# Kernel optimization log

Hardware: AMD Instinct MI355X
Metric: run time of the kernel (lower is better)

The kernel has to match this reference:

```python
import jax, jax.numpy as jnp
from jax import lax
import numpy as np

EPS = 1e-5


def _fps(xyz, S):
    B, N, _ = xyz.shape

    def step(carry, _):
        dist, far = carry  # [B,N], [B]
        c = xyz[jnp.arange(B), far]               # [B,3]
        d = jnp.sum((xyz - c[:, None, :]) ** 2, -1)  # [B,N]
        dist = jnp.minimum(dist, d)
        nxt = jnp.argmax(dist, -1).astype(jnp.int32)
        return (dist, nxt), far

    init = (jnp.full((B, N), 1e10, xyz.dtype), jnp.zeros((B,), jnp.int32))
    _, idxs = lax.scan(step, init, None, length=S)
    return jnp.transpose(idxs)  # [B,S]


def _gather(pts, idx):
    # pts: [B,N,C], idx: [B,...] -> [B,...,C]
    return jax.vmap(lambda p, i: p[i])(pts, idx)


def _conv(x, W, b):
    # 1x1 Conv1d: x [M,Cin,L], W [Cout,Cin], b [Cout]
    return jnp.einsum('mcl,oc->mol', x, W) + b[None, :, None]


def _bn(x, g, b):
    # BatchNorm1d (training-mode batch stats, biased variance)
    mu = jnp.mean(x, (0, 2), keepdims=True)
    v = jnp.var(x, (0, 2), keepdims=True)
    return g[None, :, None] * (x - mu) / jnp.sqrt(v + EPS) + b[None, :, None]


def _forward(xyz, feature, affine_alpha, affine_beta, w_tr, b_tr, g_tr, be_tr,
             w1, b1, g1, be1, w2, b2, groups, k):
    xyz = jnp.transpose(xyz, (0, 2, 1))        # [B,N,3]
    feature = jnp.transpose(feature, (0, 2, 1))  # [B,N,D]
    B, N, _ = xyz.shape
    S = groups
    xyz_ng = lax.stop_gradient(xyz)  # cluster() runs under torch.no_grad
    fps_idx = _fps(xyz_ng, S)                        # [B,S]
    new_xyz = _gather(xyz_ng, fps_idx)               # [B,S,3] (detached)
    # squared-distance kNN: [B,S,N]
    sqr = (jnp.sum(new_xyz ** 2, -1)[:, :, None]
           + jnp.sum(xyz_ng ** 2, -1)[:, None, :]
           - 2.0 * jnp.einsum('bsc,bnc->bsn', new_xyz, xyz_ng))
    _, idx = lax.top_k(-sqr, k)                      # [B,S,k] smallest distances
    new_feature = _gather(feature, fps_idx)          # [B,S,D]
    grouped_xyz = _gather(xyz, idx)                  # [B,S,k,3]
    grouped_feature = _gather(feature, idx)          # [B,S,k,D]
    grouped_feature = jnp.concatenate([grouped_feature, grouped_xyz], -1)  # [B,S,k,D+3]
    # anchor normalization
    mean = jnp.concatenate([new_feature, new_xyz], -1)[:, :, None, :]  # [B,S,1,D+3]
    diff = grouped_feature - mean
    std = jnp.std(diff.reshape(B, -1), axis=-1, ddof=1)[:, None, None, None]
    gf = affine_alpha * (diff / (std + EPS)) + affine_beta
    # concat anchor feature -> [B,S,k,2D+3]
    D = new_feature.shape[-1]
    x = jnp.concatenate([gf, jnp.broadcast_to(new_feature[:, :, None, :], (B, S, k, D))], -1)
    d = x.shape[-1]
    # PreExtraction: [B,S,k,d] -> [B*S,d,k]
    x = jnp.transpose(x, (0, 1, 3, 2)).reshape(B * S, d, k)
    x = jax.nn.relu(_bn(_conv(x, w_tr, b_tr), g_tr, be_tr))
    y = jax.nn.relu(_bn(_conv(x, w1, b1), g1, be1))
    y = _conv(y, w2, b2)
    x = jax.nn.relu(y + x)
    x = jnp.max(x, -1).reshape(B, S, -1)             # adaptive_max_pool1d(1)
    return (jnp.transpose(new_xyz, (0, 2, 1)), jnp.transpose(x, (0, 2, 1)))


def setup_inputs() -> dict:
    key = jax.random.key(0)
    k0, k1, k2, k3, k4 = jax.random.split(key, 5)
    B, N, D = 8, 4096, 64
    return {
        'xyz': jax.random.normal(k0, (B, 3, N), jnp.float32),
        'feature': jax.random.normal(k1, (B, D, N), jnp.float32),
        'affine_alpha': jnp.ones((1, 1, 1, D + 3), jnp.float32),
        'affine_beta': jnp.zeros((1, 1, 1, D + 3), jnp.float32),
        'w_tr': 0.05 * jax.random.normal(k2, (D, 3 + 2 * D), jnp.float32),
        'b_tr': jnp.zeros((D,), jnp.float32),
        'g_tr': jnp.ones((D,), jnp.float32),
        'be_tr': jnp.zeros((D,), jnp.float32),
        'w1': 0.05 * jax.random.normal(k3, (D, D), jnp.float32),
        'b1': jnp.zeros((D,), jnp.float32),
        'g1': jnp.ones((D,), jnp.float32),
        'be1': jnp.zeros((D,), jnp.float32),
        'w2': 0.05 * jax.random.normal(k4, (D, D), jnp.float32),
        'b2': jnp.zeros((D,), jnp.float32),
        'groups': 1024,
        'k': 32,
    }


def reference(xyz, feature, affine_alpha, affine_beta, w_tr, b_tr, g_tr, be_tr,
              w1, b1, g1, be1, w2, b2, groups, k):
    return _forward(xyz, feature, affine_alpha, affine_beta, w_tr, b_tr, g_tr, be_tr,
                    w1, b1, g1, be1, w2, b2, groups, k)
```

## Files before the change

### kernel.cpp

```cpp
#include <hip/hip_runtime.h>
#include <cfloat>
#include <math.h>

#define B_ 8
#define N_ 4096
#define D_ 64
#define S_ 1024
#define K_ 32
#define CIN_ 131

template <int CTRL>
__device__ __forceinline__ unsigned long long dpp_u64(unsigned long long k) {
  int lo = (int)(unsigned int)k, hi = (int)(unsigned int)(k >> 32);
  lo = __builtin_amdgcn_update_dpp(lo, lo, CTRL, 0xf, 0xf, false);
  hi = __builtin_amdgcn_update_dpp(hi, hi, CTRL, 0xf, 0xf, false);
  return ((unsigned long long)(unsigned int)hi << 32) | (unsigned int)lo;
}

__device__ __forceinline__ float wave_max_f32_dpp(float v) {
  int x = __float_as_int(v);
#define STEP(ctrl)                                                        \
  {                                                                       \
    int t = __builtin_amdgcn_update_dpp(x, x, ctrl, 0xf, 0xf, false);     \
    v = fmaxf(v, __int_as_float(t));                                      \
    x = __float_as_int(v);                                                \
  }
  STEP(0x111)
  STEP(0x112)
  STEP(0x114)
  STEP(0x118)
  STEP(0x142)
  STEP(0x143)
#undef STEP
  return __int_as_float(__builtin_amdgcn_readlane(x, 63));
}

__device__ __forceinline__ void wait_count(const unsigned int* p, unsigned int val) {
  while (__hip_atomic_load(p, __ATOMIC_ACQUIRE, __HIP_MEMORY_SCOPE_AGENT) < val)
    __builtin_amdgcn_s_sleep(8);
}
__device__ __forceinline__ void rel_add(unsigned int* p) {
  __hip_atomic_fetch_add(p, 1u, __ATOMIC_RELEASE, __HIP_MEMORY_SCOPE_AGENT);
}

__global__ __launch_bounds__(256) void stage1_kernel(
    const float* __restrict__ xyz, const float* __restrict__ feature,
    int* __restrict__ fps_idx, float* __restrict__ nxyz, float* __restrict__ out0,
    float* __restrict__ featT, int* __restrict__ knn, float* __restrict__ nfeat,
    float* __restrict__ dcache, float* __restrict__ outp,
    unsigned int* __restrict__ flags, unsigned int* __restrict__ kcount,
    unsigned int* __restrict__ gcount, unsigned int* __restrict__ tcount) {
  const int bid = blockIdx.x, tid = threadIdx.x;
  __shared__ __align__(16) float4 sp[N_];
  __shared__ int si64[64];
  __shared__ unsigned long long kbuf[2][4];

  if (bid < 8) {
    const int b = bid;
    const float* xb = xyz + (size_t)b * 3 * N_;
    const float4* xv = (const float4*)xb;
    float px[16], py[16], pz[16], dist[16];
#pragma unroll
    for (int q = 0; q < 4; q++) {
      float4 X = xv[4 * tid + q];
      float4 Y = xv[1024 + 4 * tid + q];
      float4 Z = xv[2048 + 4 * tid + q];
      px[4 * q + 0] = X.x; px[4 * q + 1] = X.y; px[4 * q + 2] = X.z; px[4 * q + 3] = X.w;
      py[4 * q + 0] = Y.x; py[4 * q + 1] = Y.y; py[4 * q + 2] = Y.z; py[4 * q + 3] = Y.w;
      pz[4 * q + 0] = Z.x; pz[4 * q + 1] = Z.y; pz[4 * q + 2] = Z.z; pz[4 * q + 3] = Z.w;
    }
#pragma unroll
    for (int i = 0; i < 16; i++) {
      dist[i] = 1e10f;
      sp[16 * tid + i] = make_float4(px[i], py[i], pz[i], 0.f);
    }
    if (tid == 0) si64[0] = 0;
    __syncthreads();
    float cx = sp[0].x, cy = sp[0].y, cz = sp[0].z;
    const int wav = tid >> 6, lane = tid & 63;
    for (int s = 1; s < S_; s++) {
      float best = -1.0f;
      int bi = 16 * tid;
#pragma unroll
      for (int i = 0; i < 16; i++) {
        float dx = __fsub_rn(px[i], cx);
        float dy = __fsub_rn(py[i], cy);
        float dz = __fsub_rn(pz[i], cz);
        float d = __fadd_rn(__fadd_rn(__fmul_rn(dx, dx), __fmul_rn(dy, dy)), __fmul_rn(dz, dz));
        dist[i] = fminf(dist[i], d);
        if (dist[i] > best) { best = dist[i]; bi = 16 * tid + i; }
      }
      float wmax = wave_max_f32_dpp(best);
      unsigned long long m = __ballot(best == wmax);
      int l = __ffsll(m) - 1;
      int widx = __builtin_amdgcn_readlane(bi, l);
      if (lane == 0)
        kbuf[s & 1][wav] =
            ((unsigned long long)(unsigned int)__float_as_int(wmax) << 32) |
            (unsigned int)(4095 - widx);
      __syncthreads();
      unsigned long long k = kbuf[s & 1][lane & 3];
      unsigned long long t;
      t = dpp_u64<0xB1>(k); if (t > k) k = t;
      t = dpp_u64<0x4E>(k); if (t > k) k = t;
      int bix = 4095 - (int)(k & 0xfffull);
      if (tid == 0) si64[s & 63] = bix;
      float4 c = sp[bix];
      cx = c.x; cy = c.y; cz = c.z;
      if ((s & 63) == 63) {
        __syncthreads();
        if (tid < 64) {
          int ss = (s - 63) + tid;
          int gs = b * S_ + ss;
          int n = si64[tid];
          float4 cc = sp[n];
          fps_idx[gs] = n;
          nxyz[(size_t)gs * 3 + 0] = cc.x;
          nxyz[(size_t)gs * 3 + 1] = cc.y;
          nxyz[(size_t)gs * 3 + 2] = cc.z;
          out0[(size_t)b * 3 * S_ + ss] = cc.x;
          out0[(size_t)b * 3 * S_ + S_ + ss] = cc.y;
          out0[(size_t)b * 3 * S_ + 2 * S_ + ss] = cc.z;
        }
        __syncthreads();
        if (tid == 0) {
          __threadfence();
          __hip_atomic_store(&flags[b * 16 + (s >> 6)], 1u, __ATOMIC_RELEASE,
                             __HIP_MEMORY_SCOPE_AGENT);
        }
      }
    }
    return;
  }
  if (bid < 520) {
    const int blk = bid - 8;
    const int b = blk >> 6, n0 = (blk & 63) * 64;
    float* tile = (float*)sp;
#pragma unroll
    for (int i = 0; i < 16; i++) {
      int c = i * 4 + (tid >> 6), nl = tid & 63;
      tile[c * 65 + nl] = feature[((size_t)b * 64 + c) * N_ + n0 + nl];
    }
    __syncthreads();
#pragma unroll
    for (int i = 0; i < 16; i++) {
      int nl = i * 4 + (tid >> 6), c = tid & 63;
      featT[((size_t)b * N_ + n0 + nl) * 64 + c] = tile[c * 65 + nl];
    }
    __syncthreads();
    if (tid == 0) rel_add(tcount);
    return;
  }
  if (bid < 8712) {
    const int bs = bid - 520;
    if (tid == 0) wait_count(&flags[bs >> 6], 1);
    __syncthreads();
    const int b = bs >> 10;
    const float* xb = xyz + (size_t)b * 3 * N_;
    const float cx = nxyz[(size_t)bs * 3], cy = nxyz[(size_t)bs * 3 + 1],
                cz = nxyz[(size_t)bs * 3 + 2];
    const float cn = __fadd_rn(__fadd_rn(__fmul_rn(cx, cx), __fmul_rn(cy, cy)), __fmul_rn(cz, cz));
    float d[16];
#pragma unroll
    for (int i = 0; i < 16; i++) {
      int n = i * 256 + tid;
      float px = xb[n], py = xb[N_ + n], pz = xb[2 * N_ + n];
      float pn = __fadd_rn(__fadd_rn(__fmul_rn(px, px), __fmul_rn(py, py)), __fmul_rn(pz, pz));
      float dot = __fadd_rn(__fadd_rn(__fmul_rn(cx, px), __fmul_rn(cy, py)), __fmul_rn(cz, pz));
      d[i] = __fsub_rn(__fadd_rn(cn, pn), __fmul_rn(2.0f, dot));
    }
    float mv = FLT_MAX;
    int mi = tid;
#pragma unroll
    for (int i = 0; i < 16; i++)
      if (d[i] < mv) { mv = d[i]; mi = i * 256 + tid; }
    int* skk = si64;
    const int wav = tid >> 6, lane = tid & 63;
    for (int j = 0; j < K_; j++) {
      unsigned int u = __float_as_uint(mv);
      u ^= ((unsigned int)((int)u >> 31) | 0x80000000u);
      unsigned long long key = ((unsigned long long)u << 32) | (unsigned int)mi;
#pragma unroll
      for (int off = 32; off >= 1; off >>= 1) {
        unsigned long long ok = __shfl_xor(key, off);
        if (ok < key) key = ok;
      }
      if (lane == 0) kbuf[j & 1][wav] = key;
      __syncthreads();
      unsigned long long kmin = kbuf[j & 1][0];
#pragma unroll
      for (int w = 1; w < 4; w++) {
        unsigned long long k2 = kbuf[j & 1][w];
        if (k2 < kmin) kmin = k2;
      }
      int g = (int)(kmin & 0xffffffffull);
      if (tid == 0) skk[j] = g;
      if ((g & 255) == tid) {
        int sl = g >> 8;
#pragma unroll
        for (int i = 0; i < 16; i++)
          if (i == sl) d[i] = FLT_MAX;
        mv = FLT_MAX; mi = tid;
#pragma unroll
        for (int i = 0; i < 16; i++)
          if (d[i] < mv) { mv = d[i]; mi = i * 256 + tid; }
      }
    }
    __syncthreads();
    if (tid < K_) knn[(size_t)bs * K_ + tid] = skk[tid];
    __syncthreads();
    if (tid == 0) rel_add(&kcount[bs >> 6]);
    return;
  }
  if (bid < 10760) {
    const int j = bid - 8712;
    if (tid == 0) {
      wait_count(tcount, 512);
      wait_count(&flags[j >> 4], 1);
    }
    __syncthreads();
    int e = j * 256 + tid;
    int bsx = e >> 6, c = e & 63;
    int bq = bsx >> 10;
    int n = fps_idx[bsx];
    nfeat[e] = featT[((size_t)bq * N_ + n) * 64 + c];
    __syncthreads();
    if (tid == 0) rel_add(&gcount[j >> 4]);
    return;
  }
  {
    const int blk = bid - 10760;
    if (tid == 0) {
      wait_count(tcount, 512);
      wait_count(&kcount[blk >> 3], 64);
      wait_count(&gcount[blk >> 3], 16);
    }
    __syncthreads();
    int* sk = si64;
    float s = 0.f, q = 0.f;
    const int c = tid & 63, qd = tid >> 6;
    for (int g = 0; g < 8; g++) {
      const int bs = blk * 8 + g, b = bs >> 10;
      if (tid < 32) sk[tid] = knn[(size_t)bs * K_ + tid];
      __syncthreads();
      float anc = nfeat[(size_t)bs * 64 + c];
#pragma unroll
      for (int it = 0; it < 8; it++) {
        int kk = it * 4 + qd;
        int n = sk[kk];
        float dd = featT[((size_t)b * N_ + n) * 64 + c] - anc;
        s += dd; q += dd * dd;
        dcache[((size_t)bs * 32 + kk) * 68 + c] = dd;
      }
      if (tid < 96) {
        int c3 = tid >> 5, kk = tid & 31;
        int n = sk[kk];
        float dd = xyz[((size_t)b * 3 + c3) * N_ + n] - nxyz[(size_t)bs * 3 + c3];
        s += dd; q += dd * dd;
        dcache[((size_t)bs * 32 + kk) * 68 + 64 + c3] = dd;
      }
      __syncthreads();
    }
#pragma unroll
    for (int off = 32; off >= 1; off >>= 1) { s += __shfl_xor(s, off); q += __shfl_xor(q, off); }
    float* rs = (float*)kbuf;
    float* rq = rs + 4;
    if ((tid & 63) == 0) { rs[tid >> 6] = s; rq[tid >> 6] = q; }
    __syncthreads();
    if (tid == 0) {
      outp[blk * 2] = rs[0] + rs[1] + rs[2] + rs[3];
      outp[blk * 2 + 1] = rq[0] + rq[1] + rq[2] + rq[3];
    }
  }
}

__global__ __launch_bounds__(256) void fps_kernel(const float* __restrict__ xyz,
                                                  int* __restrict__ fps_idx,
                                                  float* __restrict__ nxyz,
                                                  float* __restrict__ out0) {
  const int tid = threadIdx.x;
  __shared__ __align__(16) float4 sp[N_];
  __shared__ int si[S_];
  __shared__ unsigned long long keyp[2][4];
  const int b = blockIdx.x;
  const float* xb = xyz + (size_t)b * 3 * N_;
  const float4* xv = (const float4*)xb;
  float px[16], py[16], pz[16], dist[16];
#pragma unroll
  for (int q = 0; q < 4; q++) {
    float4 X = xv[4 * tid + q];
    float4 Y = xv[1024 + 4 * tid + q];
    float4 Z = xv[2048 + 4 * tid + q];
    px[4 * q + 0] = X.x; px[4 * q + 1] = X.y; px[4 * q + 2] = X.z; px[4 * q + 3] = X.w;
    py[4 * q + 0] = Y.x; py[4 * q + 1] = Y.y; py[4 * q + 2] = Y.z; py[4 * q + 3] = Y.w;
    pz[4 * q + 0] = Z.x; pz[4 * q + 1] = Z.y; pz[4 * q + 2] = Z.z; pz[4 * q + 3] = Z.w;
  }
#pragma unroll
  for (int i = 0; i < 16; i++) {
    dist[i] = 1e10f;
    sp[16 * tid + i] = make_float4(px[i], py[i], pz[i], 0.f);
  }
  if (tid == 0) si[0] = 0;
  __syncthreads();
  float cx = sp[0].x, cy = sp[0].y, cz = sp[0].z;
  const int wav = tid >> 6, lane = tid & 63;
  for (int s = 1; s < S_; s++) {
    float best = -1.0f;
    int bi = 16 * tid;
#pragma unroll
    for (int i = 0; i < 16; i++) {
      float dx = __fsub_rn(px[i], cx);
      float dy = __fsub_rn(py[i], cy);
      float dz = __fsub_rn(pz[i], cz);
      float d = __fadd_rn(__fadd_rn(__fmul_rn(dx, dx), __fmul_rn(dy, dy)), __fmul_rn(dz, dz));
      dist[i] = fminf(dist[i], d);
      if (dist[i] > best) { best = dist[i]; bi = 16 * tid + i; }
    }
    float wmax = wave_max_f32_dpp(best);
    unsigned long long m = __ballot(best == wmax);
    int l = __ffsll(m) - 1;
    int widx = __builtin_amdgcn_readlane(bi, l);
    if (lane == 0)
      keyp[s & 1][wav] =
          ((unsigned long long)(unsigned int)__float_as_int(wmax) << 32) |
          (unsigned int)(4095 - widx);
    __syncthreads();
    unsigned long long k = keyp[s & 1][lane & 3];
    unsigned long long t;
    t = dpp_u64<0xB1>(k); if (t > k) k = t;
    t = dpp_u64<0x4E>(k); if (t > k) k = t;
    int bix = 4095 - (int)(k & 0xfffull);
    if (tid == 0) si[s] = bix;
    float4 c = sp[bix];
    cx = c.x; cy = c.y; cz = c.z;
  }
  __syncthreads();
  for (int e = tid; e < S_; e += 256) {
    int n = si[e];
    fps_idx[b * S_ + e] = n;
    float4 c = sp[n];
    nxyz[(size_t)(b * S_ + e) * 3 + 0] = c.x;
    nxyz[(size_t)(b * S_ + e) * 3 + 1] = c.y;
    nxyz[(size_t)(b * S_ + e) * 3 + 2] = c.z;
    out0[(size_t)b * 3 * S_ + e] = c.x;
    out0[(size_t)b * 3 * S_ + S_ + e] = c.y;
    out0[(size_t)b * 3 * S_ + 2 * S_ + e] = c.z;
  }
}

__global__ __launch_bounds__(256) void knn_kernel(const float* __restrict__ xyz,
                                                  const float* __restrict__ nxyz,
                                                  int* __restrict__ knn) {
  const int bs = blockIdx.x, tid = threadIdx.x;
  const int b = bs >> 10;
  const float* xb = xyz + (size_t)b * 3 * N_;
  const float cx = nxyz[(size_t)bs * 3], cy = nxyz[(size_t)bs * 3 + 1], cz = nxyz[(size_t)bs * 3 + 2];
  const float cn = __fadd_rn(__fadd_rn(__fmul_rn(cx, cx), __fmul_rn(cy, cy)), __fmul_rn(cz, cz));
  float d[16];
#pragma unroll
  for (int i = 0; i < 16; i++) {
    int n = i * 256 + tid;
    float px = xb[n], py = xb[N_ + n], pz = xb[2 * N_ + n];
    float pn = __fadd_rn(__fadd_rn(__fmul_rn(px, px), __fmul_rn(py, py)), __fmul_rn(pz, pz));
    float dot = __fadd_rn(__fadd_rn(__fmul_rn(cx, px), __fmul_rn(cy, py)), __fmul_rn(cz, pz));
    d[i] = __fsub_rn(__fadd_rn(cn, pn), __fmul_rn(2.0f, dot));
  }
  float mv = FLT_MAX;
  int mi = tid;
#pragma unroll
  for (int i = 0; i < 16; i++)
    if (d[i] < mv) { mv = d[i]; mi = i * 256 + tid; }
  __shared__ unsigned long long keyp[2][4];
  __shared__ int skk[K_];
  const int wav = tid >> 6, lane = tid & 63;
  for (int j = 0; j < K_; j++) {
    unsigned int u = __float_as_uint(mv);
    u ^= ((unsigned int)((int)u >> 31) | 0x80000000u);
    unsigned long long key = ((unsigned long long)u << 32) | (unsigned int)mi;
#pragma unroll
    for (int off = 32; off >= 1; off >>= 1) {
      unsigned long long ok = __shfl_xor(key, off);
      if (ok < key) key = ok;
    }
    if (lane == 0) keyp[j & 1][wav] = key;
    __syncthreads();
    unsigned long long kmin = keyp[j & 1][0];
#pragma unroll
    for (int w = 1; w < 4; w++) {
      unsigned long long k2 = keyp[j & 1][w];
      if (k2 < kmin) kmin = k2;
    }
    int g = (int)(kmin & 0xffffffffull);
    if (tid == 0) skk[j] = g;
    if ((g & 255) == tid) {
      int sl = g >> 8;
#pragma unroll
      for (int i = 0; i < 16; i++)
        if (i == sl) d[i] = FLT_MAX;
      mv = FLT_MAX; mi = tid;
#pragma unroll
      for (int i = 0; i < 16; i++)
        if (d[i] < mv) { mv = d[i]; mi = i * 256 + tid; }
    }
  }
  __syncthreads();
  if (tid < K_) knn[(size_t)bs * K_ + tid] = skk[tid];
}

__global__ __launch_bounds__(256) void gather_nf(const float* __restrict__ feature,
                                                 const int* __restrict__ fps_i,
                                                 float* __restrict__ nfeat) {
  int e = blockIdx.x * 256 + threadIdx.x;
  int b = e >> 16, rem = e & 65535;
  int s = rem >> 6, c = rem & 63;
  int n = fps_i[b * S_ + s];
  nfeat[e] = feature[((size_t)b * 64 + c) * N_ + n];
}

__global__ __launch_bounds__(256) void std_partial(const float* __restrict__ feature,
                                                   const float* __restrict__ xyz,
                                                   const float* __restrict__ nxyz,
                                                   const float* __restrict__ nfeat,
                                                   const int* __restrict__ knn,
                                                   float* __restrict__ outp) {
  const int blk = blockIdx.x, tid = threadIdx.x;
  const int b = blk >> 6, chunk = blk & 63;
  float s = 0.f, q = 0.f;
  for (int e = tid; e < 16 * K_ * 67; e += 256) {
    int so = e / (K_ * 67);
    int rem = e - so * (K_ * 67);
    int kk = rem / 67;
    int c = rem - kk * 67;
    int bs = b * S_ + chunk * 16 + so;
    int n = knn[(size_t)bs * K_ + kk];
    float raw = (c < 64) ? feature[((size_t)b * 64 + c) * N_ + n]
                         : xyz[((size_t)b * 3 + (c - 64)) * N_ + n];
    float anc = (c < 64) ? nfeat[(size_t)bs * 64 + c]
                         : nxyz[(size_t)bs * 3 + (c - 64)];
    float dd = raw - anc;
    s += dd; q += dd * dd;
  }
#pragma unroll
  for (int off = 32; off >= 1; off >>= 1) { s += __shfl_xor(s, off); q += __shfl_xor(q, off); }
  __shared__ float rs[4], rq[4];
  if ((tid & 63) == 0) { rs[tid >> 6] = s; rq[tid >> 6] = q; }
  __syncthreads();
  if (tid == 0) {
    outp[blk * 2] = rs[0] + rs[1] + rs[2] + rs[3];
    outp[blk * 2 + 1] = rq[0] + rq[1] + rq[2] + rq[3];
  }
}

__global__ void std_final(const float* __restrict__ part, float* __restrict__ invstd) {
  int b = threadIdx.x;
  if (b < B_) {
    double s = 0.0, q = 0.0;
    for (int i = 0; i < 64; i++) {
      s += (double)part[(b * 64 + i) * 2];
      q += (double)part[(b * 64 + i) * 2 + 1];
    }
    const double n = (double)(S_ * K_ * 67);
    double var = (q - s * s / n) / (n - 1.0);
    invstd[b] = (float)(1.0 / (sqrt(var) + 1e-5));
  }
}

template <int MODE>
__global__ __launch_bounds__(256, 2) void mlp_kernel(
    const float* __restrict__ feature, const float* __restrict__ xyz,
    const float* __restrict__ nxyz, const float* __restrict__ nfeat,
    const int* __restrict__ knn, const float* __restrict__ invstd,
    const float* __restrict__ alpha, const float* __restrict__ beta,
    const float* __restrict__ w_tr, const float* __restrict__ b_tr,
    const float* __restrict__ w1, const float* __restrict__ b1,
    const float* __restrict__ w2, const float* __restrict__ b2,
    const float* __restrict__ bn_tr, const float* __restrict__ bn_1,
    float* __restrict__ bnpart, float* __restrict__ out1) {
  __shared__ __align__(16) float pool[15556];
  float* Wt = pool;
  float* xin = pool + 8516;
  float* ub = xin;
  float* tb = pool + 8516 + 4192;
  float* part = pool + 8516 + 4192 + 2304;
  int* sknn = (int*)(part + 512);
  const int bs = blockIdx.x, tid = threadIdx.x;
  const int b = bs >> 10, s = bs & 1023;
  if (tid < K_) sknn[tid] = knn[(size_t)bs * K_ + tid];
  for (int e = tid; e < 64 * 131; e += 256) {
    int o = e / 131, c = e - o * 131;
    Wt[c * 65 + o] = w_tr[e];
  }
  __syncthreads();
  const float inv = invstd[b];
  for (int e = tid; e < CIN_ * K_; e += 256) {
    int c = e >> 5, kk = e & 31;
    float v;
    if (c < 67) {
      int n = sknn[kk];
      float raw = (c < 64) ? feature[((size_t)b * 64 + c) * N_ + n]
                           : xyz[((size_t)b * 3 + (c - 64)) * N_ + n];
      float anc = (c < 64) ? nfeat[(size_t)bs * 64 + c]
                           : nxyz[(size_t)bs * 3 + (c - 64)];
      v = alpha[c] * ((raw - anc) * inv) + beta[c];
    } else {
      v = nfeat[(size_t)bs * 64 + (c - 67)];
    }
    xin[e] = v;
  }
  __syncthreads();
  const int o = tid & 63, kkb = (tid >> 6) * 8;
  float acc[8];
  {
    float bv = b_tr[o];
#pragma unroll
    for (int j = 0; j < 8; j++) acc[j] = bv;
  }
  for (int c = 0; c < CIN_; c++) {
    float w = Wt[c * 65 + o];
    const float4 xa = *(const float4*)(xin + c * 32 + kkb);
    const float4 xb4 = *(const float4*)(xin + c * 32 + kkb + 4);
    acc[0] += w * xa.x; acc[1] += w * xa.y; acc[2] += w * xa.z; acc[3] += w * xa.w;
    acc[4] += w * xb4.x; acc[5] += w * xb4.y; acc[6] += w * xb4.z; acc[7] += w * xb4.w;
  }
  if (MODE == 0) {
    float s8 = 0.f, q8 = 0.f;
#pragma unroll
    for (int j = 0; j < 8; j++) { s8 += acc[j]; q8 += acc[j] * acc[j]; }
    part[(tid >> 6) * 64 + o] = s8;
    part[256 + (tid >> 6) * 64 + o] = q8;
    __syncthreads();
    if (tid < 64) {
      float ss = 0.f, qq = 0.f;
      for (int g = 0; g < 4; g++) { ss += part[g * 64 + tid]; qq += part[256 + g * 64 + tid]; }
      bnpart[(size_t)bs * 128 + tid] = ss;
      bnpart[(size_t)bs * 128 + 64 + tid] = qq;
    }
    return;
  }
  float tv[8];
  {
    float sc = bn_tr[o], sh = bn_tr[64 + o];
#pragma unroll
    for (int j = 0; j < 8; j++) {
      tv[j] = fmaxf(fmaf(sc, acc[j], sh), 0.f);
      tb[o * 36 + kkb + j] = tv[j];
    }
  }
  __syncthreads();
  for (int e = tid; e < 64 * 64; e += 256) {
    int oo = e >> 6, c = e & 63;
    Wt[c * 65 + oo] = w1[e];
  }
  __syncthreads();
  float acc2[8];
  {
    float bv = b1[o];
#pragma unroll
    for (int j = 0; j < 8; j++) acc2[j] = bv;
  }
  for (int c = 0; c < 64; c++) {
    float w = Wt[c * 65 + o];
    const float4 ta = *(const float4*)(tb + c * 36 + kkb);
    const float4 ta2 = *(const float4*)(tb + c * 36 + kkb + 4);
    acc2[0] += w * ta.x; acc2[1] += w * ta.y; acc2[2] += w * ta.z; acc2[3] += w * ta.w;
    acc2[4] += w * ta2.x; acc2[5] += w * ta2.y; acc2[6] += w * ta2.z; acc2[7] += w * ta2.w;
  }
  if (MODE == 1) {
    float s8 = 0.f, q8 = 0.f;
#pragma unroll
    for (int j = 0; j < 8; j++) { s8 += acc2[j]; q8 += acc2[j] * acc2[j]; }
    part[(tid >> 6) * 64 + o] = s8;
    part[256 + (tid >> 6) * 64 + o] = q8;
    __syncthreads();
    if (tid < 64) {
      float ss = 0.f, qq = 0.f;
      for (int g = 0; g < 4; g++) { ss += part[g * 64 + tid]; qq += part[256 + g * 64 + tid]; }
      bnpart[(size_t)bs * 128 + tid] = ss;
      bnpart[(size_t)bs * 128 + 64 + tid] = qq;
    }
    return;
  }
  {
    float sc = bn_1[o], sh = bn_1[64 + o];
#pragma unroll
    for (int j = 0; j < 8; j++) ub[o * 36 + kkb + j] = fmaxf(fmaf(sc, acc2[j], sh), 0.f);
  }
  __syncthreads();
  for (int e = tid; e < 64 * 64; e += 256) {
    int oo = e >> 6, c = e & 63;
    Wt[c * 65 + oo] = w2[e];
  }
  __syncthreads();
  float acc3[8];
  {
    float bv = b2[o];
#pragma unroll
    for (int j = 0; j < 8; j++) acc3[j] = bv;
  }
  for (int c = 0; c < 64; c++) {
    float w = Wt[c * 65 + o];
    const float4 ua = *(const float4*)(ub + c * 36 + kkb);
    const float4 ua2 = *(const float4*)(ub + c * 36 + kkb + 4);
    acc3[0] += w * ua.x; acc3[1] += w * ua.y; acc3[2] += w * ua.z; acc3[3] += w * ua.w;
    acc3[4] += w * ua2.x; acc3[5] += w * ua2.y; acc3[6] += w * ua2.z; acc3[7] += w * ua2.w;
  }
  float m = 0.f;
#pragma unroll
  for (int j = 0; j < 8; j++) m = fmaxf(m, fmaxf(acc3[j] + tv[j], 0.f));
  part[(tid >> 6) * 64 + o] = m;
  __syncthreads();
  if (tid < 64) {
    float mm = part[tid];
    for (int g = 1; g < 4; g++) mm = fmaxf(mm, part[g * 64 + tid]);
    out1[((size_t)b * 64 + tid) * S_ + s] = mm;
  }
}

__global__ __launch_bounds__(256) void bn_finalize(const float* __restrict__ part,
                                                   const float* __restrict__ g,
                                                   const float* __restrict__ be,
                                                   float* __restrict__ bnout) {
  const int ch = blockIdx.x, tid = threadIdx.x;
  double s = 0.0, q = 0.0;
  for (int i = tid; i < B_ * S_; i += 256) {
    s += (double)part[(size_t)i * 128 + ch];
    q += (double)part[(size_t)i * 128 + 64 + ch];
  }
#pragma unroll
  for (int off = 32; off >= 1; off >>= 1) { s += __shfl_xor(s, off); q += __shfl_xor(q, off); }
  __shared__ double ls[4], lq[4];
  if ((tid & 63) == 0) { ls[tid >> 6] = s; lq[tid >> 6] = q; }
  __syncthreads();
  if (tid == 0) {
    double Ssum = ls[0] + ls[1] + ls[2] + ls[3];
    double Qsum = lq[0] + lq[1] + lq[2] + lq[3];
    const double n = (double)(B_ * S_ * K_);
    double mu = Ssum / n;
    double var = Qsum / n - mu * mu;
    double sc = (double)g[ch] / sqrt(var + 1e-5);
    bnout[ch] = (float)sc;
    bnout[64 + ch] = (float)((double)be[ch] - mu * sc);
  }
}

__global__ void std_final_c(const float* __restrict__ part, float* __restrict__ invstd) {
  int b = threadIdx.x;
  if (b < B_) {
    double s = 0.0, q = 0.0;
    for (int i = 0; i < 128; i++) {
      s += (double)part[(b * 128 + i) * 2];
      q += (double)part[(b * 128 + i) * 2 + 1];
    }
    const double n = (double)(S_ * K_ * 67);
    double var = (q - s * s / n) / (n - 1.0);
    invstd[b] = (float)(1.0 / (sqrt(var) + 1e-5));
  }
}

__global__ __launch_bounds__(256, 2) void mlp0c(
    const float* __restrict__ dcache, const float* __restrict__ nfeat,
    const float* __restrict__ invstd,
    const float* __restrict__ alpha, const float* __restrict__ beta,
    const float* __restrict__ w_tr, const float* __restrict__ b_tr,
    float* __restrict__ bnpart, float* __restrict__ tcache) {
  __shared__ __align__(16) float pool[13220];
  float* Wt = pool;
  float* xin = pool + 8516;
  float* part = pool + 8516 + 4192;
  const int bs = blockIdx.x, tid = threadIdx.x;
  const int b = bs >> 10;
  for (int e = tid; e < 64 * 131; e += 256) {
    int o = e / 131, c = e - o * 131;
    Wt[c * 65 + o] = w_tr[e];
  }
  const float inv = invstd[b];
  {
    const int c = tid & 63, qd = tid >> 6;
    float al = alpha[c], bev = beta[c];
#pragma unroll
    for (int it = 0; it < 8; it++) {
      int kk = it * 4 + qd;
      xin[c * 32 + kk] = al * (dcache[((size_t)bs * 32 + kk) * 68 + c] * inv) + bev;
    }
    if (tid < 96) {
      int c3 = 64 + (tid >> 5), kk = tid & 31;
      xin[c3 * 32 + kk] =
          alpha[c3] * (dcache[((size_t)bs * 32 + kk) * 68 + c3] * inv) + beta[c3];
    }
    for (int e = tid; e < 2048; e += 256) {
      int cc = 67 + (e >> 5), kk = e & 31;
      xin[cc * 32 + kk] = nfeat[(size_t)bs * 64 + (e >> 5)];
    }
  }
  __syncthreads();
  const int o = tid & 63, kkb = (tid >> 6) * 8;
  float acc[8];
  {
    float bv = b_tr[o];
#pragma unroll
    for (int j = 0; j < 8; j++) acc[j] = bv;
  }
  for (int c = 0; c < CIN_; c++) {
    float w = Wt[c * 65 + o];
    const float4 xa = *(const float4*)(xin + c * 32 + kkb);
    const float4 xb4 = *(const float4*)(xin + c * 32 + kkb + 4);
    acc[0] += w * xa.x; acc[1] += w * xa.y; acc[2] += w * xa.z; acc[3] += w * xa.w;
    acc[4] += w * xb4.x; acc[5] += w * xb4.y; acc[6] += w * xb4.z; acc[7] += w * xb4.w;
  }
  {
    float4* tp = (float4*)(tcache + ((size_t)bs * 64 + o) * 32 + kkb);
    tp[0] = make_float4(acc[0], acc[1], acc[2], acc[3]);
    tp[1] = make_float4(acc[4], acc[5], acc[6], acc[7]);
  }
  float s8 = 0.f, q8 = 0.f;
#pragma unroll
  for (int j = 0; j < 8; j++) { s8 += acc[j]; q8 += acc[j] * acc[j]; }
  part[(tid >> 6) * 64 + o] = s8;
  part[256 + (tid >> 6) * 64 + o] = q8;
  __syncthreads();
  if (tid < 64) {
    float ss = 0.f, qq = 0.f;
    for (int g = 0; g < 4; g++) { ss += part[g * 64 + tid]; qq += part[256 + g * 64 + tid]; }
    bnpart[(size_t)bs * 128 + tid] = ss;
    bnpart[(size_t)bs * 128 + 64 + tid] = qq;
  }
}

__global__ __launch_bounds__(256, 3) void mlp1c(
    const float* __restrict__ tcache, const float* __restrict__ bn_tr,
    const float* __restrict__ w1, const float* __restrict__ b1,
    float* __restrict__ bnpart, float* __restrict__ ucache) {
  __shared__ __align__(16) float pool[6976];
  float* Wt = pool;
  float* tb = pool + 4160;
  float* part = pool + 4160 + 2304;
  const int bs = blockIdx.x, tid = threadIdx.x;
  const int o = tid & 63, kkb = (tid >> 6) * 8;
  for (int e = tid; e < 64 * 64; e += 256) {
    int oo = e >> 6, c = e & 63;
    Wt[c * 65 + oo] = w1[e];
  }
  float t[8];
  {
    const float4* tp = (const float4*)(tcache + ((size_t)bs * 64 + o) * 32 + kkb);
    float4 a = tp[0], b4 = tp[1];
    t[0] = a.x; t[1] = a.y; t[2] = a.z; t[3] = a.w;
    t[4] = b4.x; t[5] = b4.y; t[6] = b4.z; t[7] = b4.w;
  }
  {
    float sc = bn_tr[o], sh = bn_tr[64 + o];
#pragma unroll
    for (int j = 0; j < 8; j++) tb[o * 36 + kkb + j] = fmaxf(fmaf(sc, t[j], sh), 0.f);
  }
  __syncthreads();
  float acc2[8];
  {
    float bv = b1[o];
#pragma unroll
    for (int j = 0; j < 8; j++) acc2[j] = bv;
  }
  for (int c = 0; c < 64; c++) {
    float w = Wt[c * 65 + o];
    const float4 ta = *(const float4*)(tb + c * 36 + kkb);
    const float4 ta2 = *(const float4*)(tb + c * 36 + kkb + 4);
    acc2[0] += w * ta.x; acc2[1] += w * ta.y; acc2[2] += w * ta.z; acc2[3] += w * ta.w;
    acc2[4] += w * ta2.x; acc2[5] += w * ta2.y; acc2[6] += w * ta2.z; acc2[7] += w * ta2.w;
  }
  {
    float4* up = (float4*)(ucache + ((size_t)bs * 64 + o) * 32 + kkb);
    up[0] = make_float4(acc2[0], acc2[1], acc2[2], acc2[3]);
    up[1] = make_float4(acc2[4], acc2[5], acc2[6], acc2[7]);
  }
  float s8 = 0.f, q8 = 0.f;
#pragma unroll
  for (int j = 0; j < 8; j++) { s8 += acc2[j]; q8 += acc2[j] * acc2[j]; }
  part[(tid >> 6) * 64 + o] = s8;
  part[256 + (tid >> 6) * 64 + o] = q8;
  __syncthreads();
  if (tid < 64) {
    float ss = 0.f, qq = 0.f;
    for (int g = 0; g < 4; g++) { ss += part[g * 64 + tid]; qq += part[256 + g * 64 + tid]; }
    bnpart[(size_t)bs * 128 + tid] = ss;
    bnpart[(size_t)bs * 128 + 64 + tid] = qq;
  }
}

__global__ __launch_bounds__(256, 3) void mlp2c(
    const float* __restrict__ tcache, const float* __restrict__ ucache,
    const float* __restrict__ bn_tr, const float* __restrict__ bn_1,
    const float* __restrict__ w2, const float* __restrict__ b2,
    float* __restrict__ out1) {
  __shared__ __align__(16) float pool[6976];
  float* Wt = pool;
  float* ub = pool + 4160;
  float* part = pool + 4160 + 2304;
  const int bs = blockIdx.x, tid = threadIdx.x;
  const int b = bs >> 10, s = bs & 1023;
  const int o = tid & 63, kkb = (tid >> 6) * 8;
  for (int e = tid; e < 64 * 64; e += 256) {
    int oo = e >> 6, c = e & 63;
    Wt[c * 65 + oo] = w2[e];
  }
  {
    const float4* up = (const float4*)(ucache + ((size_t)bs * 64 + o) * 32 + kkb);
    float4 a = up[0], b4 = up[1];
    float u[8] = {a.x, a.y, a.z, a.w, b4.x, b4.y, b4.z, b4.w};
    float sc = bn_1[o], sh = bn_1[64 + o];
#pragma unroll
    for (int j = 0; j < 8; j++) ub[o * 36 + kkb + j] = fmaxf(fmaf(sc, u[j], sh), 0.f);
  }
  __syncthreads();
  float acc3[8];
  {
    float bv = b2[o];
#pragma unroll
    for (int j = 0; j < 8; j++) acc3[j] = bv;
  }
  for (int c = 0; c < 64; c++) {
    float w = Wt[c * 65 + o];
    const float4 ua = *(const float4*)(ub + c * 36 + kkb);
    const float4 ua2 = *(const float4*)(ub + c * 36 + kkb + 4);
    acc3[0] += w * ua.x; acc3[1] += w * ua.y; acc3[2] += w * ua.z; acc3[3] += w * ua.w;
    acc3[4] += w * ua2.x; acc3[5] += w * ua2.y; acc3[6] += w * ua2.z; acc3[7] += w * ua2.w;
  }
  float tv[8];
  {
    const float4* tp = (const float4*)(tcache + ((size_t)bs * 64 + o) * 32 + kkb);
    float4 a = tp[0], b4 = tp[1];
    float t[8] = {a.x, a.y, a.z, a.w, b4.x, b4.y, b4.z, b4.w};
    float sc = bn_tr[o], sh = bn_tr[64 + o];
#pragma unroll
    for (int j = 0; j < 8; j++) tv[j] = fmaxf(fmaf(sc, t[j], sh), 0.f);
  }
  float m = 0.f;
#pragma unroll
  for (int j = 0; j < 8; j++) m = fmaxf(m, fmaxf(acc3[j] + tv[j], 0.f));
  part[(tid >> 6) * 64 + o] = m;
  __syncthreads();
  if (tid < 64) {
    float mm = part[tid];
    for (int g = 1; g < 4; g++) mm = fmaxf(mm, part[g * 64 + tid]);
    out1[((size_t)b * 64 + tid) * S_ + s] = mm;
  }
}

extern "C" void kernel_launch(void* const* d_in, const int* in_sizes, int n_in,
                              void* d_out, int out_size, void* d_ws, size_t ws_size,
                              hipStream_t stream) {
  const float* xyz = (const float*)d_in[0];
  const float* feature = (const float*)d_in[1];
  const float* alpha = (const float*)d_in[2];
  const float* beta = (const float*)d_in[3];
  const float* w_tr = (const float*)d_in[4];
  const float* b_tr = (const float*)d_in[5];
  const float* g_tr = (const float*)d_in[6];
  const float* be_tr = (const float*)d_in[7];
  const float* w1 = (const float*)d_in[8];
  const float* b1 = (const float*)d_in[9];
  const float* g1 = (const float*)d_in[10];
  const float* be1 = (const float*)d_in[11];
  const float* w2 = (const float*)d_in[12];
  const float* b2 = (const float*)d_in[13];

  char* ws = (char*)d_ws;
  int* fps_i = (int*)(ws);
  float* nxyz = (float*)(ws + 32768);
  float* nfeat = (float*)(ws + 131072);
  int* knn = (int*)(ws + 2228224);
  float* stdpart = (float*)(ws + 3276800);
  float* invstd = (float*)(ws + 3280896);
  float* bn_tr = (float*)(ws + 3280960);
  float* bn_1 = (float*)(ws + 3281472);
  float* bnpart = (float*)(ws + 3281984);
  float* featT = (float*)(ws + 7476288);
  float* dcache = (float*)(ws + 15864896);
  float* tcache = (float*)(ws + 87168064);
  float* ucache = (float*)(ws + 154276928);
  float* stdpart_c = (float*)(ws + 221385792);
  unsigned int* flags = (unsigned int*)(ws + 221393984);
  unsigned int* kcount = (unsigned int*)(ws + 221394496);
  unsigned int* gcount = (unsigned int*)(ws + 221395008);
  unsigned int* tcount = (unsigned int*)(ws + 221395520);

  float* out0 = (float*)d_out;
  float* out1 = out0 + B_ * 3 * S_;

  const bool big = (ws_size >= 221395584ull);

  if (big) {
    hipMemsetAsync(ws + 221393984, 0, 1600, stream);
    stage1_kernel<<<8 + 512 + 8192 + 2048 + 1024, 256, 0, stream>>>(
        xyz, feature, fps_i, nxyz, out0, featT, knn, nfeat, dcache, stdpart_c,
        flags, kcount, gcount, tcount);
    std_final_c<<<1, 64, 0, stream>>>(stdpart_c, invstd);
    mlp0c<<<B_ * S_, 256, 0, stream>>>(dcache, nfeat, invstd, alpha, beta, w_tr, b_tr,
                                       bnpart, tcache);
    bn_finalize<<<64, 256, 0, stream>>>(bnpart, g_tr, be_tr, bn_tr);
    mlp1c<<<B_ * S_, 256, 0, stream>>>(tcache, bn_tr, w1, b1, bnpart, ucache);
    bn_finalize<<<64, 256, 0, stream>>>(bnpart, g1, be1, bn_1);
    mlp2c<<<B_ * S_, 256, 0, stream>>>(tcache, ucache, bn_tr, bn_1, w2, b2, out1);
  } else {
    fps_kernel<<<8, 256, 0, stream>>>(xyz, fps_i, nxyz, out0);
    gather_nf<<<(B_ * S_ * D_) / 256, 256, 0, stream>>>(feature, fps_i, nfeat);
    knn_kernel<<<8192, 256, 0, stream>>>(xyz, nxyz, knn);
    std_partial<<<B_ * 64, 256, 0, stream>>>(feature, xyz, nxyz, nfeat, knn, stdpart);
    std_final<<<1, 64, 0, stream>>>(stdpart, invstd);
    mlp_kernel<0><<<B_ * S_, 256, 0, stream>>>(feature, xyz, nxyz, nfeat, knn, invstd,
                                               alpha, beta, w_tr, b_tr, w1, b1, w2, b2,
                                               bn_tr, bn_1, bnpart, out1);
    bn_finalize<<<64, 256, 0, stream>>>(bnpart, g_tr, be_tr, bn_tr);
    mlp_kernel<1><<<B_ * S_, 256, 0, stream>>>(feature, xyz, nxyz, nfeat, knn, invstd,
                                               alpha, beta, w_tr, b_tr, w1, b1, w2, b2,
                                               bn_tr, bn_1, bnpart, out1);
    bn_finalize<<<64, 256, 0, stream>>>(bnpart, g1, be1, bn_1);
    mlp_kernel<2><<<B_ * S_, 256, 0, stream>>>(feature, xyz, nxyz, nfeat, knn, invstd,
                                               alpha, beta, w_tr, b_tr, w1, b1, w2, b2,
                                               bn_tr, bn_1, bnpart, out1);
  }
}
```

Baseline: 1.402 ms.

## Carry FPS winner coordinates through reductions and shrink shared memory footprint

The FPS loop now tracks the coordinates of each thread's farthest point and forwards them through the wave and cross-wave reductions via LDS and DPP. This removes the per-iteration dependent LDS lookup of the chosen point, so the 64KB per-point LDS array can be dropped. Shared memory shrinks to a roughly 16KB pool, which should let more blocks of the other stages share a CU. The spin-wait also polls with relaxed loads and issues a single acquire after it exits. The trade-off is extra DPP moves and LDS stores on every FPS iteration.

```diff
diff --git a/kernel.cpp b/kernel.cpp
--- a/kernel.cpp
+++ b/kernel.cpp
@@ -15,6 +15,12 @@
   lo = __builtin_amdgcn_update_dpp(lo, lo, CTRL, 0xf, 0xf, false);
   hi = __builtin_amdgcn_update_dpp(hi, hi, CTRL, 0xf, 0xf, false);
   return ((unsigned long long)(unsigned int)hi << 32) | (unsigned int)lo;
+}
+
+template <int CTRL>
+__device__ __forceinline__ float dpp_f32(float v) {
+  int t = __builtin_amdgcn_update_dpp(__float_as_int(v), __float_as_int(v), CTRL, 0xf, 0xf, false);
+  return __int_as_float(t);
 }
 
 __device__ __forceinline__ float wave_max_f32_dpp(float v) {
@@ -36,8 +42,9 @@
 }
 
 __device__ __forceinline__ void wait_count(const unsigned int* p, unsigned int val) {
-  while (__hip_atomic_load(p, __ATOMIC_ACQUIRE, __HIP_MEMORY_SCOPE_AGENT) < val)
+  while (__hip_atomic_load(p, __ATOMIC_RELAXED, __HIP_MEMORY_SCOPE_AGENT) < val)
     __builtin_amdgcn_s_sleep(8);
+  (void)__hip_atomic_load(p, __ATOMIC_ACQUIRE, __HIP_MEMORY_SCOPE_AGENT);
 }
 __device__ __forceinline__ void rel_add(unsigned int* p) {
   __hip_atomic_fetch_add(p, 1u, __ATOMIC_RELEASE, __HIP_MEMORY_SCOPE_AGENT);
@@ -51,9 +58,11 @@
     unsigned int* __restrict__ flags, unsigned int* __restrict__ kcount,
     unsigned int* __restrict__ gcount, unsigned int* __restrict__ tcount) {
   const int bid = blockIdx.x, tid = threadIdx.x;
-  __shared__ __align__(16) float4 sp[N_];
-  __shared__ int si64[64];
-  __shared__ unsigned long long kbuf[2][4];
+  __shared__ __align__(16) float pool[4160];
+  float4* scoord64 = (float4*)pool;
+  int* si64 = (int*)(pool + 256);
+  unsigned long long* kbuf = (unsigned long long*)(pool + 320);
+  float4* cbuf = (float4*)(pool + 336);
 
   if (bid < 8) {
     const int b = bid;
@@ -70,17 +79,19 @@
       pz[4 * q + 0] = Z.x; pz[4 * q + 1] = Z.y; pz[4 * q + 2] = Z.z; pz[4 * q + 3] = Z.w;
     }
 #pragma unroll
-    for (int i = 0; i < 16; i++) {
-      dist[i] = 1e10f;
-      sp[16 * tid + i] = make_float4(px[i], py[i], pz[i], 0.f);
-    }
-    if (tid == 0) si64[0] = 0;
-    __syncthreads();
-    float cx = sp[0].x, cy = sp[0].y, cz = sp[0].z;
+    for (int i = 0; i < 16; i++) dist[i] = 1e10f;
+    if (tid == 0) {
+      si64[0] = 0;
+      scoord64[0] = make_float4(px[0], py[0], pz[0], 0.f);
+    }
+    __syncthreads();
+    float4 c0 = scoord64[0];
+    float cx = c0.x, cy = c0.y, cz = c0.z;
     const int wav = tid >> 6, lane = tid & 63;
     for (int s = 1; s < S_; s++) {
       float best = -1.0f;
       int bi = 16 * tid;
+      float bx = px[0], by = py[0], bz = pz[0];
 #pragma unroll
       for (int i = 0; i < 16; i++) {
         float dx = __fsub_rn(px[i], cx);
@@ -88,39 +99,51 @@
         float dz = __fsub_rn(pz[i], cz);
         float d = __fadd_rn(__fadd_rn(__fmul_rn(dx, dx), __fmul_rn(dy, dy)), __fmul_rn(dz, dz));
         dist[i] = fminf(dist[i], d);
-        if (dist[i] > best) { best = dist[i]; bi = 16 * tid + i; }
+        if (dist[i] > best) {
+          best = dist[i]; bi = 16 * tid + i;
+          bx = px[i]; by = py[i]; bz = pz[i];
+        }
       }
       float wmax = wave_max_f32_dpp(best);
       unsigned long long m = __ballot(best == wmax);
       int l = __ffsll(m) - 1;
-      int widx = __builtin_amdgcn_readlane(bi, l);
-      if (lane == 0)
-        kbuf[s & 1][wav] =
-            ((unsigned long long)(unsigned int)__float_as_int(wmax) << 32) |
-            (unsigned int)(4095 - widx);
+      if (lane == l) {
+        kbuf[(s & 1) * 4 + wav] =
+            ((unsigned long long)(unsigned int)__float_as_int(best) << 32) |
+            (unsigned int)(4095 - bi);
+        cbuf[(s & 1) * 4 + wav] = make_float4(bx, by, bz, 0.f);
+      }
       __syncthreads();
-      unsigned long long k = kbuf[s & 1][lane & 3];
-      unsigned long long t;
-      t = dpp_u64<0xB1>(k); if (t > k) k = t;
-      t = dpp_u64<0x4E>(k); if (t > k) k = t;
+      unsigned long long k = kbuf[(s & 1) * 4 + (lane & 3)];
+      float4 cc = cbuf[(s & 1) * 4 + (lane & 3)];
+      {
+        unsigned long long t = dpp_u64<0xB1>(k);
+        float tx = dpp_f32<0xB1>(cc.x), ty = dpp_f32<0xB1>(cc.y), tz = dpp_f32<0xB1>(cc.z);
+        if (t > k) { k = t; cc.x = tx; cc.y = ty; cc.z = tz; }
+        t = dpp_u64<0x4E>(k);
+        tx = dpp_f32<0x4E>(cc.x); ty = dpp_f32<0x4E>(cc.y); tz = dpp_f32<0x4E>(cc.z);
+        if (t > k) { k = t; cc.x = tx; cc.y = ty; cc.z = tz; }
+      }
       int bix = 4095 - (int)(k & 0xfffull);
-      if (tid == 0) si64[s & 63] = bix;
-      float4 c = sp[bix];
-      cx = c.x; cy = c.y; cz = c.z;
+      cx = cc.x; cy = cc.y; cz = cc.z;
+      if (tid == 0) {
+        si64[s & 63] = bix;
+        scoord64[s & 63] = make_float4(cx, cy, cz, 0.f);
+      }
       if ((s & 63) == 63) {
         __syncthreads();
         if (tid < 64) {
           int ss = (s - 63) + tid;
           int gs = b * S_ + ss;
           int n = si64[tid];
-          float4 cc = sp[n];
+          float4 cc2 = scoord64[tid];
           fps_idx[gs] = n;
-          nxyz[(size_t)gs * 3 + 0] = cc.x;
-          nxyz[(size_t)gs * 3 + 1] = cc.y;
-          nxyz[(size_t)gs * 3 + 2] = cc.z;
-          out0[(size_t)b * 3 * S_ + ss] = cc.x;
-          out0[(size_t)b * 3 * S_ + S_ + ss] = cc.y;
-          out0[(size_t)b * 3 * S_ + 2 * S_ + ss] = cc.z;
+          nxyz[(size_t)gs * 3 + 0] = cc2.x;
+          nxyz[(size_t)gs * 3 + 1] = cc2.y;
+          nxyz[(size_t)gs * 3 + 2] = cc2.z;
+          out0[(size_t)b * 3 * S_ + ss] = cc2.x;
+          out0[(size_t)b * 3 * S_ + S_ + ss] = cc2.y;
+          out0[(size_t)b * 3 * S_ + 2 * S_ + ss] = cc2.z;
         }
         __syncthreads();
         if (tid == 0) {
@@ -135,7 +158,7 @@
   if (bid < 520) {
     const int blk = bid - 8;
     const int b = blk >> 6, n0 = (blk & 63) * 64;
-    float* tile = (float*)sp;
+    float* tile = pool;
 #pragma unroll
     for (int i = 0; i < 16; i++) {
       int c = i * 4 + (tid >> 6), nl = tid & 63;
@@ -185,12 +208,12 @@
         unsigned long long ok = __shfl_xor(key, off);
         if (ok < key) key = ok;
       }
-      if (lane == 0) kbuf[j & 1][wav] = key;
+      if (lane == 0) kbuf[(j & 1) * 4 + wav] = key;
       __syncthreads();
-      unsigned long long kmin = kbuf[j & 1][0];
+      unsigned long long kmin = kbuf[(j & 1) * 4];
 #pragma unroll
       for (int w = 1; w < 4; w++) {
-        unsigned long long k2 = kbuf[j & 1][w];
+        unsigned long long k2 = kbuf[(j & 1) * 4 + w];
         if (k2 < kmin) kmin = k2;
       }
       int g = (int)(kmin & 0xffffffffull);
```

After: 1.509 ms. 7.6% more time.
